# Optimization experiments

Hardware: AMD Instinct MI355X
Metric: run time of the kernel (lower is better)

The kernel has to match this reference:

```python
import jax, jax.numpy as jnp
import numpy as np

EPS = 1e-5  # BatchNorm eps (ME.MinkowskiBatchNorm default)


def setup_inputs() -> dict:
    key = jax.random.key(0)
    k1, k2, k3, k4 = jax.random.split(key, 4)
    N, Cin, Cout, K = 65536, 256, 128, 8  # K = kernel_size**dimension = 2**3
    x = jax.random.normal(k1, (N, Cin), dtype=jnp.float32)
    W = jax.random.normal(k2, (K, Cin, Cout), dtype=jnp.float32) * 0.02
    gamma = jax.random.uniform(k3, (Cout,), dtype=jnp.float32, minval=0.5, maxval=1.5)
    beta = jax.random.normal(k4, (Cout,), dtype=jnp.float32) * 0.1
    return {"x": x, "W": W, "gamma": gamma, "beta": beta}


def reference(x, W, gamma, beta):
    # Transpose Minkowski conv, kernel=2, stride=2, dim=3: each input voxel
    # emits 2^3 = 8 disjoint child voxels; child for offset k gets x @ W[k].
    # Kernel map is identity per offset (no scatter-add collisions because
    # kernel_size == stride), so outputs stack to [8*N, Cout].
    Cout = W.shape[-1]
    out = jnp.einsum('nc,kcd->knd', x, W).reshape(-1, Cout)  # [8N, Cout]
    # MinkowskiBatchNorm over all active output sites (training batch stats).
    mean = jnp.mean(out, axis=0)
    var = jnp.mean(jnp.square(out - mean), axis=0)  # biased var, as BN uses
    y = (out - mean) * jax.lax.rsqrt(var + EPS) * gamma + beta
    return jnp.maximum(y, 0.0)  # MinkowskiReLU
```

## Files before the change

kernel.cpp:

```cpp
#include <hip/hip_runtime.h>
#include <stdint.h>

#define N_ROWS 65536
#define CIN 256
#define COUT 128

typedef __bf16 bf16x8 __attribute__((ext_vector_type(8)));
typedef float f32x4 __attribute__((ext_vector_type(4)));
typedef unsigned short u16;
typedef unsigned int u32;

__device__ __forceinline__ float truncbf(float f) {
  u32 x = __builtin_bit_cast(u32, f) & 0xFFFF0000u;
  return __builtin_bit_cast(float, x);
}
__device__ __forceinline__ u32 packbf(float a, float b) {
  return __builtin_amdgcn_perm(__builtin_bit_cast(u32, b),
                               __builtin_bit_cast(u32, a), 0x07060302u);
}

__device__ __forceinline__ void async_ld16(const float* g, float* l) {
  __builtin_amdgcn_global_load_lds((const __attribute__((address_space(1))) u32*)g,
                                   (__attribute__((address_space(3))) u32*)l,
                                   16, 0, 0);
}

__global__ __launch_bounds__(512, 2) void gram_partial(const float* __restrict__ x,
                                                       float* __restrict__ part,
                                                       float* __restrict__ colsum) {
  __shared__ u32 xT[256 * 18];
  const int tid = threadIdx.x, lane = tid & 63;
  const int w = tid >> 6;
  const int wm = w >> 2, wn = w & 3;
  const int q = lane >> 4, r = lane & 15;
  const int row0 = blockIdx.x * 512;
  const int cpair = tid & 127, c0 = cpair * 2;
  const int npb = tid >> 7;

  f32x4 acc[8][4];
  #pragma unroll
  for (int i = 0; i < 8; ++i)
    #pragma unroll
    for (int j = 0; j < 4; ++j) acc[i][j] = (f32x4){0.f, 0.f, 0.f, 0.f};
  float cs0 = 0.f, cs1 = 0.f;

  for (int ch = 0; ch < 16; ++ch) {
    const int r0 = row0 + ch * 32;
    #pragma unroll
    for (int i = 0; i < 4; ++i) {
      int np = npb + i * 4;
      int n0 = r0 + np * 2;
      float2 g0 = *(const float2*)&x[(size_t)n0 * CIN + c0];
      float2 g1 = *(const float2*)&x[(size_t)(n0 + 1) * CIN + c0];
      xT[18 * c0 + np] = packbf(g0.x, g1.x);
      xT[18 * (c0 + 1) + np] = packbf(g0.y, g1.y);
      cs0 += truncbf(g0.x) + truncbf(g1.x);
      cs1 += truncbf(g0.y) + truncbf(g1.y);
    }
    __syncthreads();
    bf16x8 af[8], bfr[4];
    #pragma unroll
    for (int mt = 0; mt < 8; ++mt) {
      int c = wm * 128 + mt * 16 + r;
      union { u32 d[4]; bf16x8 v; } t;
      const u32* p = &xT[18 * c + 4 * q];
      t.d[0] = p[0]; t.d[1] = p[1]; t.d[2] = p[2]; t.d[3] = p[3];
      af[mt] = t.v;
    }
    #pragma unroll
    for (int nt = 0; nt < 4; ++nt) {
      int c = wn * 64 + nt * 16 + r;
      union { u32 d[4]; bf16x8 v; } t;
      const u32* p = &xT[18 * c + 4 * q];
      t.d[0] = p[0]; t.d[1] = p[1]; t.d[2] = p[2]; t.d[3] = p[3];
      bfr[nt] = t.v;
    }
    #pragma unroll
    for (int mt = 0; mt < 8; ++mt)
      #pragma unroll
      for (int nt = 0; nt < 4; ++nt)
        acc[mt][nt] = __builtin_amdgcn_mfma_f32_16x16x32_bf16(af[mt], bfr[nt], acc[mt][nt], 0, 0, 0);
    __syncthreads();
  }

  float* pb = part + (size_t)blockIdx.x * 65536;
  #pragma unroll
  for (int mt = 0; mt < 8; ++mt)
    #pragma unroll
    for (int nt = 0; nt < 4; ++nt)
      #pragma unroll
      for (int i = 0; i < 4; ++i) {
        int row = wm * 128 + mt * 16 + q * 4 + i;
        int col = wn * 64 + nt * 16 + r;
        pb[row * 256 + col] = acc[mt][nt][i];
      }
  atomicAdd(&colsum[c0], cs0);
  atomicAdd(&colsum[c0 + 1], cs1);
}

__global__ void gram_reduce(const float* __restrict__ part, float* __restrict__ G) {
  int idx = (blockIdx.x * 256 + threadIdx.x) * 4;
  float s0 = 0.f, s1 = 0.f, s2 = 0.f, s3 = 0.f;
  for (int b = 0; b < 128; ++b) {
    float4 v = *(const float4*)(part + (size_t)b * 65536 + idx);
    s0 += v.x; s1 += v.y; s2 += v.z; s3 += v.w;
  }
  float4 o; o.x = s0; o.y = s1; o.z = s2; o.w = s3;
  *(float4*)(G + idx) = o;
}

__global__ __launch_bounds__(256) void stats_kernel(const float* __restrict__ G,
                                                    const float* __restrict__ colsum,
                                                    const float* __restrict__ W,
                                                    const float* __restrict__ gamma,
                                                    const float* __restrict__ beta,
                                                    float* __restrict__ scale,
                                                    float* __restrict__ bias) {
  const int d = blockIdx.x;
  const int t = threadIdx.x;
  __shared__ float wv[256][8];
  __shared__ float rr[16];
  float wt[8];
  #pragma unroll
  for (int k = 0; k < 8; ++k) wt[k] = truncbf(W[((size_t)k * CIN + t) * COUT + d]);
  #pragma unroll
  for (int k = 0; k < 8; ++k) wv[t][k] = wt[k];
  __syncthreads();

  float q = 0.f;
  for (int j = 0; j < 256; ++j) {
    float g = G[j * 256 + t];
    float dot = 0.f;
    #pragma unroll
    for (int k = 0; k < 8; ++k) dot += wv[j][k] * wt[k];
    q += g * dot;
  }
  float wsum = 0.f;
  #pragma unroll
  for (int k = 0; k < 8; ++k) wsum += wt[k];
  float m = colsum[t] * wsum;

  #pragma unroll
  for (int off = 32; off; off >>= 1) {
    q += __shfl_down(q, off, 64);
    m += __shfl_down(m, off, 64);
  }
  int wid = t >> 6;
  if ((t & 63) == 0) { rr[wid] = q; rr[wid + 8] = m; }
  __syncthreads();
  if (t == 0) {
    float qt = rr[0] + rr[1] + rr[2] + rr[3];
    float mn = rr[8] + rr[9] + rr[10] + rr[11];
    const float invM = 1.f / 524288.f;
    float mean = mn * invM;
    float var = qt * invM - mean * mean;
    float s = gamma[d] * rsqrtf(var + 1e-5f);
    scale[d] = s;
    bias[d] = beta[d] - mean * s;
  }
}

__global__ void wtrans_kernel(const float* __restrict__ W, u16* __restrict__ Wt) {
  __shared__ u16 tile[32][128];
  const int blk = blockIdx.x, t = threadIdx.x;
  const int k = blk >> 3, cb = blk & 7;
  #pragma unroll
  for (int i = 0; i < 4; ++i) {
    int u = t + i * 256;
    int ci = u >> 5, d4 = (u & 31) * 4;
    float4 f = *(const float4*)&W[((size_t)k * CIN + cb * 32 + ci) * COUT + d4];
    uint2 p; p.x = packbf(f.x, f.y); p.y = packbf(f.z, f.w);
    *(uint2*)&tile[ci][d4] = p;
  }
  __syncthreads();
  #pragma unroll
  for (int i = 0; i < 2; ++i) {
    int v = t + i * 256;
    int d = v >> 2, c0 = (v & 3) * 8;
    union { u16 s[8]; uint4 u4; } p;
    #pragma unroll
    for (int j = 0; j < 8; ++j) p.s[j] = tile[c0 + j][d];
    *(uint4*)&Wt[((size_t)blk * 128 + d) * 32 + c0] = p.u4;
  }
}

__global__ __launch_bounds__(256, 2) void gemm_kernel(const float* __restrict__ x,
                                                      const u16* __restrict__ Wt,
                                                      const float* __restrict__ scale,
                                                      const float* __restrict__ bias,
                                                      float* __restrict__ out) {
  __shared__ float As[4096];
  const int tid = threadIdx.x, lane = tid & 63;
  const int w = tid >> 6, wr = w >> 1, wc = w & 1;
  const int q = lane >> 4, r = lane & 15;
  const int k = blockIdx.x & 7;
  const int m0 = (blockIdx.x >> 3) * 128;

  const u16* wbase = Wt + (size_t)k * 8 * 4096;
  const int boff = (wc * 64 + r) * 32 + q * 8;

  bf16x8 bcur[4], bnext[4];
  #pragma unroll
  for (int nt = 0; nt < 4; ++nt)
    bcur[nt] = *(const bf16x8*)&wbase[boff + nt * 512];

  f32x4 acc[4][4];
  #pragma unroll
  for (int i = 0; i < 4; ++i)
    #pragma unroll
    for (int j = 0; j < 4; ++j) acc[i][j] = (f32x4){0.f, 0.f, 0.f, 0.f};

  for (int cb = 0; cb < 8; ++cb) {
    #pragma unroll
    for (int i = 0; i < 4; ++i) {
      int u = tid + i * 256;
      int row = u >> 3;
      int s = (u & 7) ^ (row & 7);
      const float* g = x + (size_t)(m0 + row) * CIN + cb * 32 + s * 4;
      float* l = As + (w * 64 + i * 256) * 4;
      async_ld16(g, l);
    }
    if (cb < 7) {
      #pragma unroll
      for (int nt = 0; nt < 4; ++nt)
        bnext[nt] = *(const bf16x8*)&wbase[(cb + 1) * 4096 + boff + nt * 512];
    }
    __syncthreads();
    bf16x8 af[4];
    #pragma unroll
    for (int mt = 0; mt < 4; ++mt) {
      int row = wr * 64 + mt * 16 + r;
      union { u32 d[4]; bf16x8 v; } t;
      #pragma unroll
      for (int b = 0; b < 2; ++b) {
        int unit = row * 8 + ((2 * q + b) ^ (row & 7));
        float4 f = *(const float4*)&As[unit * 4];
        t.d[b * 2 + 0] = packbf(f.x, f.y);
        t.d[b * 2 + 1] = packbf(f.z, f.w);
      }
      af[mt] = t.v;
    }
    #pragma unroll
    for (int mt = 0; mt < 4; ++mt)
      #pragma unroll
      for (int nt = 0; nt < 4; ++nt)
        acc[mt][nt] = __builtin_amdgcn_mfma_f32_16x16x32_bf16(af[mt], bcur[nt], acc[mt][nt], 0, 0, 0);
    __syncthreads();
    if (cb < 7) {
      #pragma unroll
      for (int nt = 0; nt < 4; ++nt) bcur[nt] = bnext[nt];
    }
  }

  float sv[4], bv[4];
  #pragma unroll
  for (int nt = 0; nt < 4; ++nt) {
    int col = wc * 64 + nt * 16 + r;
    sv[nt] = scale[col]; bv[nt] = bias[col];
  }
  #pragma unroll
  for (int mt = 0; mt < 4; ++mt) {
    if (mt) __syncthreads();
    #pragma unroll
    for (int nt = 0; nt < 4; ++nt)
      #pragma unroll
      for (int i = 0; i < 4; ++i) {
        int rl = wr * 16 + q * 4 + i;
        int col = wc * 64 + nt * 16 + r;
        float y = acc[mt][nt][i] * sv[nt] + bv[nt];
        y = y > 0.f ? y : 0.f;
        As[rl * 128 + col] = y;
      }
    __syncthreads();
    #pragma unroll
    for (int i = 0; i < 4; ++i) {
      int u = tid + i * 256;
      int rl = u >> 5, off = (u & 31) * 4;
      int grow = m0 + (rl >> 4) * 64 + mt * 16 + (rl & 15);
      *(float4*)&out[((size_t)k * N_ROWS + grow) * COUT + off] =
          *(const float4*)&As[rl * 128 + off];
    }
  }
}

extern "C" void kernel_launch(void* const* d_in, const int* in_sizes, int n_in,
                              void* d_out, int out_size, void* d_ws, size_t ws_size,
                              hipStream_t stream) {
  const float* x = (const float*)d_in[0];
  const float* W = (const float*)d_in[1];
  const float* gamma = (const float*)d_in[2];
  const float* beta = (const float*)d_in[3];
  float* out = (float*)d_out;

  float* ws = (float*)d_ws;
  float* G = ws;
  float* colsum = ws + 65536;
  float* scale = ws + 65792;
  float* bias = ws + 65920;
  u16* Wt = (u16*)(ws + 66048);

  float* part = (float*)d_out;

  hipMemsetAsync(colsum, 0, 256 * sizeof(float), stream);
  gram_partial<<<128, 512, 0, stream>>>(x, part, colsum);
  gram_reduce<<<64, 256, 0, stream>>>(part, G);
  stats_kernel<<<128, 256, 0, stream>>>(G, colsum, W, gamma, beta, scale, bias);
  wtrans_kernel<<<64, 256, 0, stream>>>(W, Wt);
  gemm_kernel<<<4096, 256, 0, stream>>>(x, Wt, scale, bias, out);
}
```

Before: 454.5 us.

## Emit bf16 copy of x during Gram pass and reuse it across all 8 offsets in GEMM

The Gram pass now also writes a bf16 copy of x to workspace. A new GEMM kernel loads a 128-row bf16 tile of x into LDS once and loops over all 8 weight offsets, instead of re-reading fp32 x per offset. This cuts global reads of x and the fp32-to-bf16 conversion in the main GEMM. It also doubles the Gram grid to 256 blocks, reduces colsum atomics through shared memory, and writes output directly without LDS staging, which risks less coalesced stores. The fp32 path remains as a fallback when the workspace is too small.

```diff
diff --git a/kernel.cpp b/kernel.cpp
--- a/kernel.cpp
+++ b/kernel.cpp
@@ -19,21 +19,24 @@
                                __builtin_bit_cast(u32, a), 0x07060302u);
 }
 
-__device__ __forceinline__ void async_ld16(const float* g, float* l) {
+__device__ __forceinline__ void async_ld16(const void* g, void* l) {
   __builtin_amdgcn_global_load_lds((const __attribute__((address_space(1))) u32*)g,
                                    (__attribute__((address_space(3))) u32*)l,
                                    16, 0, 0);
 }
 
+template <bool EMIT_XB>
 __global__ __launch_bounds__(512, 2) void gram_partial(const float* __restrict__ x,
                                                        float* __restrict__ part,
-                                                       float* __restrict__ colsum) {
+                                                       float* __restrict__ colsum,
+                                                       u32* __restrict__ xb) {
   __shared__ u32 xT[256 * 18];
+  __shared__ float cs_s[4][256];
   const int tid = threadIdx.x, lane = tid & 63;
   const int w = tid >> 6;
   const int wm = w >> 2, wn = w & 3;
   const int q = lane >> 4, r = lane & 15;
-  const int row0 = blockIdx.x * 512;
+  const int row0 = blockIdx.x * 256;
   const int cpair = tid & 127, c0 = cpair * 2;
   const int npb = tid >> 7;
 
@@ -44,7 +47,7 @@
     for (int j = 0; j < 4; ++j) acc[i][j] = (f32x4){0.f, 0.f, 0.f, 0.f};
   float cs0 = 0.f, cs1 = 0.f;
 
-  for (int ch = 0; ch < 16; ++ch) {
+  for (int ch = 0; ch < 8; ++ch) {
     const int r0 = row0 + ch * 32;
     #pragma unroll
     for (int i = 0; i < 4; ++i) {
@@ -54,6 +57,10 @@
       float2 g1 = *(const float2*)&x[(size_t)(n0 + 1) * CIN + c0];
       xT[18 * c0 + np] = packbf(g0.x, g1.x);
       xT[18 * (c0 + 1) + np] = packbf(g0.y, g1.y);
+      if (EMIT_XB) {
+        xb[(size_t)n0 * 128 + cpair] = packbf(g0.x, g0.y);
+        xb[(size_t)(n0 + 1) * 128 + cpair] = packbf(g1.x, g1.y);
+      }
       cs0 += truncbf(g0.x) + truncbf(g1.x);
       cs1 += truncbf(g0.y) + truncbf(g1.y);
     }
@@ -94,19 +101,19 @@
         int col = wn * 64 + nt * 16 + r;
         pb[row * 256 + col] = acc[mt][nt][i];
       }
-  atomicAdd(&colsum[c0], cs0);
-  atomicAdd(&colsum[c0 + 1], cs1);
+
+  cs_s[npb][c0] = cs0;
+  cs_s[npb][c0 + 1] = cs1;
+  __syncthreads();
+  if (tid < 256)
+    atomicAdd(&colsum[tid], cs_s[0][tid] + cs_s[1][tid] + cs_s[2][tid] + cs_s[3][tid]);
 }
 
 __global__ void gram_reduce(const float* __restrict__ part, float* __restrict__ G) {
-  int idx = (blockIdx.x * 256 + threadIdx.x) * 4;
-  float s0 = 0.f, s1 = 0.f, s2 = 0.f, s3 = 0.f;
-  for (int b = 0; b < 128; ++b) {
-    float4 v = *(const float4*)(part + (size_t)b * 65536 + idx);
-    s0 += v.x; s1 += v.y; s2 += v.z; s3 += v.w;
-  }
-  float4 o; o.x = s0; o.y = s1; o.z = s2; o.w = s3;
-  *(float4*)(G + idx) = o;
+  int g = blockIdx.x * 256 + threadIdx.x;
+  float s = 0.f;
+  for (int b = 0; b < 256; ++b) s += part[(size_t)b * 65536 + g];
+  G[g] = s;
 }
 
 __global__ __launch_bounds__(256) void stats_kernel(const float* __restrict__ G,
@@ -184,12 +191,93 @@
   }
 }
 
-__global__ __launch_bounds__(256, 2) void gemm_kernel(const float* __restrict__ x,
-                                                      const u16* __restrict__ Wt,
-                                                      const float* __restrict__ scale,
-                                                      const float* __restrict__ bias,
-                                                      float* __restrict__ out) {
-  __shared__ float As[4096];
+__global__ __launch_bounds__(256, 2) void gemm_xb(const u16* __restrict__ xb,
+                                                  const u16* __restrict__ Wt,
+                                                  const float* __restrict__ scale,
+                                                  const float* __restrict__ bias,
+                                                  float* __restrict__ out) {
+  __shared__ u16 As[32768];
+  const int tid = threadIdx.x, lane = tid & 63;
+  const int w = tid >> 6, wr = w >> 1, wc = w & 1;
+  const int q = lane >> 4, r = lane & 15;
+  const int m0 = blockIdx.x * 128;
+
+  #pragma unroll
+  for (int i = 0; i < 16; ++i) {
+    int u = tid + i * 256;
+    int cb = u >> 9, row = (u >> 2) & 127, seg = u & 3;
+    const u16* g = xb + (size_t)(m0 + row) * CIN + cb * 32 + seg * 8;
+    async_ld16(g, As + (size_t)u * 8);
+  }
+
+  float sv[4], bv[4];
+  #pragma unroll
+  for (int nt = 0; nt < 4; ++nt) {
+    int col = wc * 64 + nt * 16 + r;
+    sv[nt] = scale[col]; bv[nt] = bias[col];
+  }
+
+  const int boff = (wc * 64 + r) * 32 + q * 8;
+  bf16x8 bcur[4], bnext[4];
+  #pragma unroll
+  for (int nt = 0; nt < 4; ++nt)
+    bcur[nt] = *(const bf16x8*)&Wt[boff + nt * 512];
+
+  __syncthreads();
+
+  int j = 0;
+  for (int k = 0; k < 8; ++k) {
+    f32x4 acc[4][4];
+    #pragma unroll
+    for (int i = 0; i < 4; ++i)
+      #pragma unroll
+      for (int jj = 0; jj < 4; ++jj) acc[i][jj] = (f32x4){0.f, 0.f, 0.f, 0.f};
+
+    #pragma unroll
+    for (int cb = 0; cb < 8; ++cb) {
+      if (j < 63) {
+        #pragma unroll
+        for (int nt = 0; nt < 4; ++nt)
+          bnext[nt] = *(const bf16x8*)&Wt[(size_t)(j + 1) * 4096 + boff + nt * 512];
+      }
+      bf16x8 af[4];
+      #pragma unroll
+      for (int mt = 0; mt < 4; ++mt)
+        af[mt] = *(const bf16x8*)&As[((cb * 128) + wr * 64 + mt * 16 + r) * 32 + q * 8];
+      #pragma unroll
+      for (int mt = 0; mt < 4; ++mt)
+        #pragma unroll
+        for (int nt = 0; nt < 4; ++nt)
+          acc[mt][nt] = __builtin_amdgcn_mfma_f32_16x16x32_bf16(af[mt], bcur[nt], acc[mt][nt], 0, 0, 0);
+      if (j < 63) {
+        #pragma unroll
+        for (int nt = 0; nt < 4; ++nt) bcur[nt] = bnext[nt];
+      }
+      ++j;
+    }
+
+    const size_t obase = (size_t)k * N_ROWS + m0;
+    #pragma unroll
+    for (int mt = 0; mt < 4; ++mt)
+      #pragma unroll
+      for (int nt = 0; nt < 4; ++nt)
+        #pragma unroll
+        for (int i = 0; i < 4; ++i) {
+          int grow = wr * 64 + mt * 16 + q * 4 + i;
+          int col = wc * 64 + nt * 16 + r;
+          float y = acc[mt][nt][i] * sv[nt] + bv[nt];
+          y = y > 0.f ? y : 0.f;
+          out[(obase + grow) * COUT + col] = y;
+        }
+  }
+}
+
+__global__ __launch_bounds__(256, 2) void gemm_fp32(const float* __restrict__ x,
+                                                    const u16* __restrict__ Wt,
+                                                    const float* __restrict__ scale,
+                                                    const float* __restrict__ bias,
+                                                    float* __restrict__ out) {
+  __shared__ float Asf[4096];
   const int tid = threadIdx.x, lane = tid & 63;
   const int w = tid >> 6, wr = w >> 1, wc = w & 1;
   const int q = lane >> 4, r = lane & 15;
@@ -217,8 +305,7 @@
       int row = u >> 3;
       int s = (u & 7) ^ (row & 7);
       const float* g = x + (size_t)(m0 + row) * CIN + cb * 32 + s * 4;
-      float* l = As + (w * 64 + i * 256) * 4;
-      async_ld16(g, l);
+      async_ld16(g, Asf + (w * 64 + i * 256) * 4);
     }
     if (cb < 7) {
       #pragma unroll
@@ -234,7 +321,7 @@
       #pragma unroll
       for (int b = 0; b < 2; ++b) {
         int unit = row * 8 + ((2 * q + b) ^ (row & 7));
-        float4 f = *(const float4*)&As[unit * 4];
+        float4 f = *(const float4*)&Asf[unit * 4];
         t.d[b * 2 + 0] = packbf(f.x, f.y);
         t.d[b * 2 + 1] = packbf(f.z, f.w);
       }
@@ -258,29 +345,19 @@
     int col = wc * 64 + nt * 16 + r;
     sv[nt] = scale[col]; bv[nt] = bias[col];
   }
-  #pragma unroll
-  for (int mt = 0; mt < 4; ++mt) {
-    if (mt) __syncthreads();
+  const size_t obase = (size_t)k * N_ROWS + m0;
+  #pragma unroll
+  for (int mt = 0; mt < 4; ++mt)
     #pragma unroll
     for (int nt = 0; nt < 4; ++nt)
       #pragma unroll
       for (int i = 0; i < 4; ++i) {
-        int rl = wr * 16 + q * 4 + i;
+        int grow = wr * 64 + mt * 16 + q * 4 + i;
         int col = wc * 64 + nt * 16 + r;
         float y = acc[mt][nt][i] * sv[nt] + bv[nt];
         y = y > 0.f ? y : 0.f;
-        As[rl * 128 + col] = y;
-      }
-    __syncthreads();
-    #pragma unroll
-    for (int i = 0; i < 4; ++i) {
-      int u = tid + i * 256;
-      int rl = u >> 5, off = (u & 31) * 4;
-      int grow = m0 + (rl >> 4) * 64 + mt * 16 + (rl & 15);
-      *(float4*)&out[((size_t)k * N_ROWS + grow) * COUT + off] =
-          *(const float4*)&As[rl * 128 + off];
-    }
-  }
+        out[(obase + grow) * COUT + col] = y;
+      }
 }
 
 extern "C" void kernel_launch(void* const* d_in, const int* in_sizes, int n_in,
@@ -298,13 +375,24 @@
   float* scale = ws + 65792;
   float* bias = ws + 65920;
   u16* Wt = (u16*)(ws + 66048);
+  u32* xb = (u32*)((char*)d_ws + (1 << 20));
+  const size_t need = (1u << 20) + (size_t)N_ROWS * CIN * 2;
+  const bool big_ws = ws_size >= need;
 
   float* part = (float*)d_out;
 
   hipMemsetAsync(colsum, 0, 256 * sizeof(float), stream);
-  gram_partial<<<128, 512, 0, stream>>>(x, part, colsum);
-  gram_reduce<<<64, 256, 0, stream>>>(part, G);
+  if (big_ws) {
+    gram_partial<true><<<256, 512, 0, stream>>>(x, part, colsum, xb);
+  } else {
+    gram_partial<false><<<256, 512, 0, stream>>>(x, part, colsum, xb);
+  }
+  gram_reduce<<<256, 256, 0, stream>>>(part, G);
   stats_kernel<<<128, 256, 0, stream>>>(G, colsum, W, gamma, beta, scale, bias);
   wtrans_kernel<<<64, 256, 0, stream>>>(W, Wt);
-  gemm_kernel<<<4096, 256, 0, stream>>>(x, Wt, scale, bias, out);
-}
+  if (big_ws) {
+    gemm_xb<<<512, 256, 0, stream>>>((const u16*)xb, Wt, scale, bias, out);
+  } else {
+    gemm_fp32<<<4096, 256, 0, stream>>>(x, Wt, scale, bias, out);
+  }
+}
```

Result: faster. 393.1 us (-13.5%).
